# Kernel tuning notes

Measured on AMD Instinct MI355X. Metric: run time of the kernel, lower is better.

The kernel has to match this reference:

```python
import jax, jax.numpy as jnp
import numpy as np

N_HEADS = 16
DIM = 1024
DPH = DIM // N_HEADS  # 64
NEG_INF = -1e20       # neginf(float32) in the torch source


def setup_inputs() -> dict:
    key0 = jax.random.key(0)
    ks = jax.random.split(key0, 12)
    bs, qlen, nrev, klen = 32, 128, 20, 64
    w = lambda k: jax.random.normal(k, (DIM, DIM), jnp.float32) * 0.02
    return {
        "query": jax.random.normal(ks[0], (bs, qlen, DIM), jnp.float32),
        "key": jax.random.normal(ks[1], (bs, nrev, klen, DIM), jnp.float32),
        "value": jax.random.normal(ks[2], (bs, nrev, klen, DIM), jnp.float32),
        "mask": jax.random.randint(ks[3], (bs, nrev), 0, 2, jnp.int32),
        "mask2": jax.random.randint(ks[4], (bs, nrev, klen), 0, 2, jnp.int32),
        "Wq": w(ks[5]), "bq": jnp.zeros((DIM,), jnp.float32),
        "Wk": w(ks[6]), "bk": jnp.zeros((DIM,), jnp.float32),
        "Wv": w(ks[7]), "bv": jnp.zeros((DIM,), jnp.float32),
        "Wo": w(ks[8]), "bo": jnp.zeros((DIM,), jnp.float32),
        "sa_a": jax.random.normal(ks[9], (DPH, DPH), jnp.float32) * 0.1,
        "sa_b": jax.random.normal(ks[10], (DPH, 1), jnp.float32) * 0.1,
    }


def _forward(query, key, value, mask, mask2,
             Wq, bq, Wk, bk, Wv, bv, Wo, bo, sa_a, sa_b):
    bs, qlen, dim = query.shape
    _, nrev, klen, _ = key.shape
    dph = dim // N_HEADS
    scale = float(dph) ** 0.5

    # linear projections + head split (torch Linear: x @ W.T + b)
    q = (query @ Wq.T + bq).reshape(bs, qlen, N_HEADS, dph)        # [B,Q,H,d]
    k = (key @ Wk.T + bk).reshape(bs, nrev, klen, N_HEADS, dph)    # [B,R,T,H,d]
    v = (value @ Wv.T + bv).reshape(bs, nrev, klen, N_HEADS, dph)  # [B,R,T,H,d]

    # --- token-level attention: per review, q attends over review tokens ---
    scores = jnp.einsum('bqhd,brthd->bhrqt', q, k) / scale          # [B,H,R,Q,T]
    tok_pad = (mask2 == 0)[:, None, :, None, :]                     # [B,1,R,1,T]
    scores = jnp.where(tok_pad, NEG_INF, scores)
    attn_w = jax.nn.softmax(scores, axis=-1)
    att = jnp.einsum('bhrqt,brthd->bhqrd', attn_w, v)               # [B,H,Q,R,d]

    # --- review-level self-attention pooling (SelfAttentionSeq) ---
    # e = tanh(h @ a) @ b ; mask applied only if some reviews have mask==0,
    # and then NONZERO mask positions get -1e30 (faithful to the source).
    e = jnp.tanh(att @ sa_a) @ sa_b                                 # [B,H,Q,R,1]
    e = e[..., 0]                                                   # [B,H,Q,R]
    mf = mask.astype(att.dtype)                                     # [B,R]
    any_zero = (jnp.sum(mask == 0, axis=-1, keepdims=True) > 0).astype(att.dtype)  # [B,1]
    add_mask = (-1e30 * mf) * any_zero                              # [B,R]
    e = e + add_mask[:, None, None, :]
    rev_w = jax.nn.softmax(e, axis=-1)                              # [B,H,Q,R]
    pooled = jnp.einsum('bhqr,bhqrd->bhqd', rev_w, att)             # [B,H,Q,d]

    # merge heads + output projection
    merged = pooled.transpose(0, 2, 1, 3).reshape(bs, qlen, dim)    # [B,Q,D]
    return merged @ Wo.T + bo


def reference(query, key, value, mask, mask2,
              Wq, bq, Wk, bk, Wv, bv, Wo, bo, sa_a, sa_b):
    return _forward(query, key, value, mask, mask2,
                    Wq, bq, Wk, bk, Wv, bv, Wo, bo, sa_a, sa_b)
```

## Files before the change

### kernel.cpp

```cpp
#include <hip/hip_runtime.h>
#include <stdint.h>


typedef __attribute__((ext_vector_type(8))) short bf16x8;
typedef __attribute__((ext_vector_type(4))) float f32x4;
typedef __attribute__((ext_vector_type(4))) unsigned int u32x4;
typedef __attribute__((address_space(1))) const unsigned int as1_t;
typedef __attribute__((address_space(3))) unsigned int as3_t;

#define DEVI static __device__ __forceinline__

DEVI unsigned short f2bf(float f) {
  unsigned int u = __float_as_uint(f);
  u += 0x7fffu + ((u >> 16) & 1u);
  return (unsigned short)(u >> 16);
}
DEVI unsigned int pack2(float a, float b) {
  return (unsigned int)f2bf(a) | ((unsigned int)f2bf(b) << 16);
}
DEVI unsigned int cvtpk(float a, float b) {
  unsigned int r;
  asm("v_cvt_pk_bf16_f32 %0, %1, %2" : "=v"(r) : "v"(a), "v"(b));
  return r;
}

DEVI void gload_lds16(const void* g, void* l) {
  __builtin_amdgcn_global_load_lds((as1_t*)g, (as3_t*)l, 16, 0, 0);
}

DEVI float fast_tanh(float x) {
  float ax = fabsf(x);
  float e = __expf(2.0f * ax);
  float r = __builtin_fmaf(-2.0f, __builtin_amdgcn_rcpf(e + 1.0f), 1.0f);
  return copysignf(r, x);
}

__global__ __launch_bounds__(256) void prep(
    const float* __restrict__ w0, const float* __restrict__ w1,
    const float* __restrict__ w2, const float* __restrict__ w3,
    unsigned short* __restrict__ o0, unsigned short* __restrict__ o1,
    unsigned short* __restrict__ o2, unsigned short* __restrict__ o3,
    const float* __restrict__ qsrc, unsigned short* __restrict__ qdst,
    const int* __restrict__ mask, int* __restrict__ cmp) {
  const int bx = (int)blockIdx.x;
  const int tid = (int)threadIdx.x;
  if (bx < 1024) {
    const int i = bx * 256 + tid;
    f32x4 v;
    uint2 a;
    v = ((const f32x4*)w0)[i]; a.x = pack2(v[0], v[1]); a.y = pack2(v[2], v[3]);
    *(uint2*)(o0 + 4 * (size_t)i) = a;
    v = ((const f32x4*)w1)[i]; a.x = pack2(v[0], v[1]); a.y = pack2(v[2], v[3]);
    *(uint2*)(o1 + 4 * (size_t)i) = a;
    v = ((const f32x4*)w2)[i]; a.x = pack2(v[0], v[1]); a.y = pack2(v[2], v[3]);
    *(uint2*)(o2 + 4 * (size_t)i) = a;
    v = ((const f32x4*)w3)[i]; a.x = pack2(v[0], v[1]); a.y = pack2(v[2], v[3]);
    *(uint2*)(o3 + 4 * (size_t)i) = a;
  } else if (bx < 2048) {
    const int i = (bx - 1024) * 256 + tid;
#pragma unroll
    for (int h = 0; h < 2; ++h) {
      const int u = i + h * 262144;
      f32x4 a = ((const f32x4*)qsrc)[2 * u];
      f32x4 b = ((const f32x4*)qsrc)[2 * u + 1];
      u32x4 o = {pack2(a[0], a[1]), pack2(a[2], a[3]),
                 pack2(b[0], b[1]), pack2(b[2], b[3])};
      ((u32x4*)qdst)[u] = o;
    }
  } else {
    __shared__ int azs[32];
    if (tid < 32) {
      int z = 0;
#pragma unroll
      for (int r = 0; r < 20; ++r) z |= (mask[tid * 20 + r] == 0) ? 1 : 0;
      azs[tid] = z;
    }
    __syncthreads();
    if (tid < 64) {
      const int lane = tid;
      int base = 0;
      int lasts = 0;
      for (int it = 0; it < 10; ++it) {
        const int s = it * 64 + lane;
        const int bb = s / 20;
        const int actv = azs[bb] ? ((mask[s] == 0) ? 1 : 0) : 1;
        unsigned long long bal = __ballot(actv);
        const int off = (int)__popcll(bal & ((1ull << lane) - 1ull));
        if (actv) {
          cmp[1 + base + off] = s;
          lasts = s;
        }
        base += (int)__popcll(bal);
      }
#pragma unroll
      for (int d = 1; d < 64; d <<= 1) {
        int o = __shfl_xor(lasts, d);
        lasts = lasts > o ? lasts : o;
      }
      if (lane == 0) {
        cmp[0] = base;
        cmp[1 + base] = lasts;
      }
    }
  }
}

__global__ void cvt_act(const float* __restrict__ src,
                        unsigned short* __restrict__ dst,
                        const int* __restrict__ cmp) {
  const int cnt = cmp[0];
  const int n = ((cnt + 1) & ~1) * 8192;
  const int stride = (int)(gridDim.x * blockDim.x);
  for (int u = (int)(blockIdx.x * blockDim.x + threadIdx.x); u < n; u += stride) {
    const int s = u >> 13;
    const int e = u & 8191;
    const size_t so = (size_t)cmp[1 + s] * 65536 + (size_t)e * 8;
    f32x4 a = *(const f32x4*)(src + so);
    f32x4 b = *(const f32x4*)(src + so + 4);
    u32x4 o = {pack2(a[0], a[1]), pack2(a[2], a[3]),
               pack2(b[0], b[1]), pack2(b[2], b[3])};
    *(u32x4*)(dst + (size_t)u * 8) = o;
  }
}

template <int OUT_MODE, int ADT, int SC, int CMP>
__global__ __launch_bounds__(256, 4) void gemm_bt(
    const void* __restrict__ Ain, const unsigned short* __restrict__ W,
    const float* __restrict__ bias, void* __restrict__ Cout, int N, int K, int nnt,
    const int* __restrict__ cmp) {
  __shared__ __align__(16) char smem[32768];
  char* Asb = smem;
  char* Bsb = smem + 16384;
  const int tid = (int)threadIdx.x;
  const int lane = tid & 63, wave = tid >> 6;
  const int lm = lane & 15, l4 = lane >> 4;
  const int nb = (int)gridDim.x;
  const int bx = (int)blockIdx.x;
  const int wr = wave >> 1, wc = wave & 1;

  int mt, nt, cs0, cs1;
  if (CMP) {
    const int cnt = cmp[0];
    const int tiles = (cnt + 1) >> 1;
    if (bx >= tiles * 8) return;
    const int lg = (bx & 7) * tiles + (bx >> 3);
    mt = lg / nnt;
    nt = lg % nnt;
    cs0 = cmp[1 + 2 * mt];
    cs1 = cmp[2 + 2 * mt];
  } else {
    const int lg = (bx & 7) * (nb >> 3) + (bx >> 3);
    mt = lg / nnt;
    nt = lg % nnt;
    cs0 = 2 * mt;
    cs1 = 2 * mt + 1;
  }

  f32x4 zero4 = {0.f, 0.f, 0.f, 0.f};
  f32x4 acc[4][4];
#pragma unroll
  for (int i = 0; i < 4; ++i)
#pragma unroll
    for (int j = 0; j < 4; ++j) acc[i][j] = zero4;

  const int srow = tid >> 2, sblk = tid & 3;
  const int scb = sblk ^ ((srow >> 1) & 3);
  const unsigned short* wpg = W + (size_t)(nt * 128 + srow) * K + scb * 8;
  const int kx = (lm >> 1) & 3;

  const unsigned short* apg =
      (const unsigned short*)Ain + (size_t)(mt * 128 + srow) * K + scb * 8;
  const int NT = K >> 5;
#pragma unroll
  for (int t0 = 0; t0 < 2; ++t0) {
    const int kt = t0 * 32;
    gload_lds16(apg + kt, Asb + t0 * 8192 + tid * 16);
    gload_lds16(apg + (size_t)64 * K + kt, Asb + t0 * 8192 + 4096 + tid * 16);
    gload_lds16(wpg + kt, Bsb + t0 * 8192 + tid * 16);
    gload_lds16(wpg + (size_t)64 * K + kt, Bsb + t0 * 8192 + 4096 + tid * 16);
  }
  int cur = 0;
  for (int t = 0; t < NT; ++t) {
    if (t + 1 < NT)
      asm volatile("s_waitcnt vmcnt(4)" ::: "memory");
    else
      asm volatile("s_waitcnt vmcnt(0)" ::: "memory");
    asm volatile("s_barrier" ::: "memory");
    bf16x8 af[4], bfr[4];
#pragma unroll
    for (int i = 0; i < 4; ++i)
      af[i] = *(const bf16x8*)(Asb + cur * 8192 + (wr * 64 + i * 16 + lm) * 64 +
                               ((l4 ^ kx) * 16));
#pragma unroll
    for (int j = 0; j < 4; ++j)
      bfr[j] = *(const bf16x8*)(Bsb + cur * 8192 + (wc * 64 + j * 16 + lm) * 64 +
                                ((l4 ^ kx) * 16));
#pragma unroll
    for (int i = 0; i < 4; ++i)
#pragma unroll
      for (int j = 0; j < 4; ++j)
        acc[i][j] = __builtin_amdgcn_mfma_f32_16x16x32_bf16(af[i], bfr[j], acc[i][j], 0, 0, 0);
    asm volatile("s_barrier" ::: "memory");
    if (t + 2 < NT) {
      const int kt = (t + 2) * 32;
      gload_lds16(apg + kt, Asb + cur * 8192 + tid * 16);
      gload_lds16(apg + (size_t)64 * K + kt, Asb + cur * 8192 + 4096 + tid * 16);
      gload_lds16(wpg + kt, Bsb + cur * 8192 + tid * 16);
      gload_lds16(wpg + (size_t)64 * K + kt, Bsb + cur * 8192 + 4096 + tid * 16);
    }
    cur ^= 1;
  }

  const int c0o = nt * 128 + wc * 64 + lm;
  float bb[4];
#pragma unroll
  for (int j = 0; j < 4; ++j) bb[j] = bias[c0o + j * 16];
  const int mslot = wr ? cs1 : cs0;

  if (OUT_MODE < 2) {
#pragma unroll
    for (int i = 0; i < 4; ++i)
#pragma unroll
      for (int j = 0; j < 4; ++j)
#pragma unroll
        for (int p = 0; p < 4; ++p) {
          size_t grow = (size_t)mslot * 64 + (l4 * 4 + i * 16 + p);
          size_t idx = grow * N + (size_t)(c0o + j * 16);
          float v = acc[i][j][p] + bb[j];
          if (SC) v *= 0.125f;
          if (OUT_MODE == 1)
            ((unsigned short*)Cout)[idx] = f2bf(v);
          else
            ((float*)Cout)[idx] = v;
        }
  } else {
    const int hh = (nt * 128 + wc * 64) / 64;
    unsigned short* vt = (unsigned short*)Cout;
    const size_t base = ((size_t)mslot * 16 + hh) * 4096;
#pragma unroll
    for (int j = 0; j < 4; ++j) {
      const int d = lm + j * 16;
#pragma unroll
      for (int i = 0; i < 4; ++i) {
        uint2 wv;
        wv.x = pack2(acc[i][j][0] + bb[j], acc[i][j][1] + bb[j]);
        wv.y = pack2(acc[i][j][2] + bb[j], acc[i][j][3] + bb[j]);
        *(uint2*)(vt + base + (size_t)d * 64 + i * 16 + l4 * 4) = wv;
      }
    }
  }
}

__global__ __launch_bounds__(512, 4) void attn2(
    const unsigned short* __restrict__ qb, const unsigned short* __restrict__ kb,
    const unsigned short* __restrict__ vtg, const int* __restrict__ mask,
    const int* __restrict__ mask2, const float* __restrict__ sa_a,
    const float* __restrict__ sa_b, unsigned short* __restrict__ merged) {
  const int h = (int)blockIdx.x;
  const int b = (int)blockIdx.y;
  const int tid = (int)threadIdx.x;
  const int lane = tid & 63, wave = tid >> 6;
  const int lm = lane & 15, l4 = lane >> 4;
  const int sw = (lm & 7) << 4;

  __shared__ unsigned short kv_s[2][2][64 * 64];
  __shared__ unsigned short pa_s[8 * 16 * 64];

  char* kvb0 = (char*)kv_s;
  char* qreg = (char*)kv_s + 16384;
  char* satb = (char*)pa_s;

  unsigned am = 0u;
#pragma unroll
  for (int rr = 0; rr < 20; ++rr)
    am |= (mask[b * 20 + rr] == 0) ? (1u << rr) : 0u;
  const unsigned act = am ? am : 0xFFFFFu;

#pragma unroll
  for (int s = 0; s < 2; ++s) {
    int idx = s * 512 + tid, row = idx >> 3, blk = idx & 7;
    int cb = blk ^ (row & 7);
    gload_lds16(qb + (size_t)(b * 128 + row) * 1024 + h * 64 + cb * 8, qreg + idx * 16);
  }
#pragma unroll
  for (int s = 0; s < 8; ++s) {
    int idx = s * 512 + tid, jj = idx & 63, d = idx >> 6;
    *(unsigned short*)(satb + jj * 128 + ((d * 2) ^ ((jj & 7) << 4))) =
        f2bf(sa_a[d * 64 + jj]);
  }
  const int srow = tid >> 3, sblk = tid & 7;
  const int scb = sblk ^ (srow & 7);
  int r = (int)__builtin_ctz(act);
  unsigned rem = act & (act - 1u);
  gload_lds16(kb + ((size_t)(b * 20 + r) * 64 + srow) * 1024 + h * 64 + scb * 8,
              kvb0 + tid * 16);
  gload_lds16(vtg + ((size_t)(b * 20 + r) * 16 + h) * 4096 + srow * 64 + scb * 8,
              kvb0 + 8192 + tid * 16);

  f32x4 sbv[4];
#pragma unroll
  for (int i = 0; i < 4; ++i) sbv[i] = *(const f32x4*)(sa_b + i * 16 + l4 * 4);

  __syncthreads();

  const char* qrp = qreg + (wave * 16 + lm) * 128;
  bf16x8 qf[2];
  qf[0] = *(const bf16x8*)(qrp + ((l4 * 16) ^ sw));
  qf[1] = *(const bf16x8*)(qrp + ((64 + l4 * 16) ^ sw));
  bf16x8 sfr[2][4];
#pragma unroll
  for (int kk = 0; kk < 2; ++kk)
#pragma unroll
    for (int i = 0; i < 4; ++i)
      sfr[kk][i] = *(const bf16x8*)(satb + (i * 16 + lm) * 128 +
                                    ((kk * 64 + l4 * 16) ^ sw));
  asm volatile("s_waitcnt lgkmcnt(0)" ::: "memory");
  __syncthreads();

  char* pw = (char*)pa_s + wave * 2048 + lm * 128;

  f32x4 zero4 = {0.f, 0.f, 0.f, 0.f};
  f32x4 Pacc[4];
#pragma unroll
  for (int i = 0; i < 4; ++i) Pacc[i] = zero4;
  float m_run = -3.0e38f, s_run = 0.0f;

  int it = 0;
  for (;;) {
    const int pb = it & 1;
    if (it) __syncthreads();
    const int nr = rem ? (int)__builtin_ctz(rem) : -1;
    if (nr >= 0) {
      const int nbuf = pb ^ 1;
      gload_lds16(kb + ((size_t)(b * 20 + nr) * 64 + srow) * 1024 + h * 64 + scb * 8,
                  kvb0 + nbuf * 16384 + tid * 16);
      gload_lds16(vtg + ((size_t)(b * 20 + nr) * 16 + h) * 4096 + srow * 64 + scb * 8,
                  kvb0 + nbuf * 16384 + 8192 + tid * 16);
    }
    const char* kbse = kvb0 + pb * 16384;
    const char* vbse = kvb0 + pb * 16384 + 8192;

    const int mbase = (b * 20 + r) * 64;
    int4 m2v[4];
#pragma unroll
    for (int i = 0; i < 4; ++i)
      m2v[i] = *(const int4*)(mask2 + mbase + i * 16 + l4 * 4);

    f32x4 sc[4];
#pragma unroll
    for (int i = 0; i < 4; ++i) sc[i] = zero4;
    __builtin_amdgcn_s_setprio(1);
#pragma unroll
    for (int kk = 0; kk < 2; ++kk) {
      bf16x8 kf[4];
#pragma unroll
      for (int i = 0; i < 4; ++i)
        kf[i] = *(const bf16x8*)(kbse + (i * 16 + lm) * 128 + ((kk * 64 + l4 * 16) ^ sw));
#pragma unroll
      for (int i = 0; i < 4; ++i)
        sc[i] = __builtin_amdgcn_mfma_f32_16x16x32_bf16(kf[i], qf[kk], sc[i], 0, 0, 0);
    }
    __builtin_amdgcn_s_setprio(0);

#pragma unroll
    for (int i = 0; i < 4; ++i) {
      sc[i][0] = (m2v[i].x == 0) ? -1e20f : sc[i][0];
      sc[i][1] = (m2v[i].y == 0) ? -1e20f : sc[i][1];
      sc[i][2] = (m2v[i].z == 0) ? -1e20f : sc[i][2];
      sc[i][3] = (m2v[i].w == 0) ? -1e20f : sc[i][3];
    }
    float mx = sc[0][0];
#pragma unroll
    for (int i = 0; i < 4; ++i)
#pragma unroll
      for (int p = 0; p < 4; ++p) mx = fmaxf(mx, sc[i][p]);
    mx = fmaxf(mx, __shfl_xor(mx, 16));
    mx = fmaxf(mx, __shfl_xor(mx, 32));
    float sum = 0.f;
#pragma unroll
    for (int i = 0; i < 4; ++i)
#pragma unroll
      for (int p = 0; p < 4; ++p) {
        float e = __expf(sc[i][p] - mx);
        sc[i][p] = e;
        sum += e;
      }
    sum += __shfl_xor(sum, 16);
    sum += __shfl_xor(sum, 32);
    const float pinv = __builtin_amdgcn_rcpf(sum);

#pragma unroll
    for (int i = 0; i < 4; ++i) {
      uint2 wv;
      wv.x = cvtpk(sc[i][0] * pinv, sc[i][1] * pinv);
      wv.y = cvtpk(sc[i][2] * pinv, sc[i][3] * pinv);
      *(uint2*)(pw + ((i * 32 + l4 * 8) ^ sw)) = wv;
    }

    f32x4 av[4];
#pragma unroll
    for (int i = 0; i < 4; ++i) av[i] = zero4;
    __builtin_amdgcn_s_setprio(1);
#pragma unroll
    for (int kk = 0; kk < 2; ++kk) {
      bf16x8 pf = *(const bf16x8*)(pw + ((kk * 64 + l4 * 16) ^ sw));
      bf16x8 vf[4];
#pragma unroll
      for (int i = 0; i < 4; ++i)
        vf[i] = *(const bf16x8*)(vbse + (i * 16 + lm) * 128 + ((kk * 64 + l4 * 16) ^ sw));
#pragma unroll
      for (int i = 0; i < 4; ++i)
        av[i] = __builtin_amdgcn_mfma_f32_16x16x32_bf16(vf[i], pf, av[i], 0, 0, 0);
    }
    __builtin_amdgcn_s_setprio(0);

#pragma unroll
    for (int i = 0; i < 4; ++i) {
      uint2 wv;
      wv.x = cvtpk(av[i][0], av[i][1]);
      wv.y = cvtpk(av[i][2], av[i][3]);
      *(uint2*)(pw + ((i * 32 + l4 * 8) ^ sw)) = wv;
    }

    f32x4 ep[4];
#pragma unroll
    for (int i = 0; i < 4; ++i) ep[i] = zero4;
    __builtin_amdgcn_s_setprio(1);
#pragma unroll
    for (int kk = 0; kk < 2; ++kk) {
      bf16x8 afr = *(const bf16x8*)(pw + ((kk * 64 + l4 * 16) ^ sw));
#pragma unroll
      for (int i = 0; i < 4; ++i)
        ep[i] = __builtin_amdgcn_mfma_f32_16x16x32_bf16(sfr[kk][i], afr, ep[i], 0, 0, 0);
    }
    __builtin_amdgcn_s_setprio(0);
    float a = 0.f;
#pragma unroll
    for (int i = 0; i < 4; ++i)
#pragma unroll
      for (int p = 0; p < 4; ++p) a += fast_tanh(ep[i][p]) * sbv[i][p];
    a += __shfl_xor(a, 16);
    a += __shfl_xor(a, 32);

    const float e_r = a;
    const float mnew = fmaxf(m_run, e_r);
    const float scl = __expf(m_run - mnew);
    const float w = __expf(e_r - mnew);
    s_run = s_run * scl + w;
#pragma unroll
    for (int i = 0; i < 4; ++i)
#pragma unroll
      for (int p = 0; p < 4; ++p) Pacc[i][p] = Pacc[i][p] * scl + w * av[i][p];
    m_run = mnew;

    if (nr < 0) break;
    r = nr;
    rem &= rem - 1u;
    ++it;
  }

  const float inv_s = __builtin_amdgcn_rcpf(s_run);
  unsigned short* mrow = merged + (size_t)(b * 128 + wave * 16 + lm) * 1024 + h * 64;
#pragma unroll
  for (int i = 0; i < 4; ++i) {
    uint2 o;
    o.x = cvtpk(Pacc[i][0] * inv_s, Pacc[i][1] * inv_s);
    o.y = cvtpk(Pacc[i][2] * inv_s, Pacc[i][3] * inv_s);
    *(uint2*)(mrow + i * 16 + l4 * 4) = o;
  }
}

extern "C" void kernel_launch(void* const* d_in, const int* in_sizes, int n_in,
                              void* d_out, int out_size, void* d_ws, size_t ws_size,
                              hipStream_t stream) {
  (void)in_sizes; (void)n_in; (void)out_size; (void)ws_size;
  const float* query = (const float*)d_in[0];
  const float* key   = (const float*)d_in[1];
  const float* value = (const float*)d_in[2];
  const int*   mask  = (const int*)d_in[3];
  const int*   mask2 = (const int*)d_in[4];
  const float* Wq = (const float*)d_in[5];
  const float* bq = (const float*)d_in[6];
  const float* Wk = (const float*)d_in[7];
  const float* bk = (const float*)d_in[8];
  const float* Wv = (const float*)d_in[9];
  const float* bv = (const float*)d_in[10];
  const float* Wo = (const float*)d_in[11];
  const float* bo = (const float*)d_in[12];
  const float* sa_a = (const float*)d_in[13];
  const float* sa_b = (const float*)d_in[14];

  char* ws = (char*)d_ws;
  size_t off = 0;
  auto carve = [&](size_t bytes) -> char* {
    char* p = ws + off;
    off += (bytes + 255) & ~(size_t)255;
    return p;
  };
  unsigned short* wq_b = (unsigned short*)carve((size_t)1024 * 1024 * 2);
  unsigned short* wk_b = (unsigned short*)carve((size_t)1024 * 1024 * 2);
  unsigned short* wv_b = (unsigned short*)carve((size_t)1024 * 1024 * 2);
  unsigned short* wo_b = (unsigned short*)carve((size_t)1024 * 1024 * 2);
  unsigned short* q_b  = (unsigned short*)carve((size_t)4096 * 1024 * 2);
  unsigned short* k_b  = (unsigned short*)carve((size_t)40960 * 1024 * 2);
  unsigned short* vt_g = (unsigned short*)carve((size_t)40960 * 1024 * 2);
  unsigned short* mrg  = (unsigned short*)carve((size_t)4096 * 1024 * 2);
  int* cmp = (int*)carve(4096);
  unsigned short* act = (unsigned short*)carve((size_t)40960 * 1024 * 2);

  prep<<<2049, 256, 0, stream>>>(Wq, Wk, Wv, Wo, wq_b, wk_b, wv_b, wo_b,
                                 query, act, mask, cmp);

  gemm_bt<1, 1, 1, 0><<<dim3(32 * 8), 256, 0, stream>>>(act, wq_b, bq, q_b, 1024, 1024, 8, cmp);

  cvt_act<<<2048, 256, 0, stream>>>(key, act, cmp);
  gemm_bt<1, 1, 0, 1><<<dim3(320 * 8), 256, 0, stream>>>(act, wk_b, bk, k_b, 1024, 1024, 8, cmp);

  cvt_act<<<2048, 256, 0, stream>>>(value, act, cmp);
  gemm_bt<2, 1, 0, 1><<<dim3(320 * 8), 256, 0, stream>>>(act, wv_b, bv, vt_g, 1024, 1024, 8, cmp);

  attn2<<<dim3(16, 32), 512, 0, stream>>>(q_b, k_b, vt_g, mask, mask2, sa_a, sa_b, mrg);

  gemm_bt<0, 1, 0, 0><<<dim3(32 * 8), 256, 0, stream>>>(mrg, wo_b, bo, d_out, 1024, 1024, 8, cmp);
}
```

Baseline: 259.0 us.

## Fuse key conversion into prep, merge Q/K GEMMs, use sparse in-place activation layout

Active reviews are no longer compacted into a dense buffer. The key and value conversions now write bf16 rows in place at their original slot offsets and skip inactive reviews using a per-block mask bitmap. The GEMM gathers the two 64-row halves of each tile through the compacted slot list. The key conversion moves into the prep launch and the Q and K projections share one launch, which cuts kernel launches and lets the small Q GEMM overlap the K GEMM. The cost is a larger prep grid, a separate Q activation buffer, and a loop in which every thread iterates over all 640 slots even when most are inactive.

```diff
diff --git a/kernel.cpp b/kernel.cpp
--- a/kernel.cpp
+++ b/kernel.cpp
@@ -33,6 +33,34 @@
   float e = __expf(2.0f * ax);
   float r = __builtin_fmaf(-2.0f, __builtin_amdgcn_rcpf(e + 1.0f), 1.0f);
   return copysignf(r, x);
+}
+
+DEVI void cvt_sparse_body(const float* __restrict__ src,
+                          unsigned short* __restrict__ dst,
+                          const unsigned char* actb, int gid, int stride) {
+  for (int u = gid; u < 640 * 8192; u += stride) {
+    const int s = u >> 13;
+    if (!actb[s]) continue;
+    f32x4 a = *(const f32x4*)(src + (size_t)u * 8);
+    f32x4 b = *(const f32x4*)(src + (size_t)u * 8 + 4);
+    u32x4 o = {pack2(a[0], a[1]), pack2(a[2], a[3]),
+               pack2(b[0], b[1]), pack2(b[2], b[3])};
+    *(u32x4*)(dst + (size_t)u * 8) = o;
+  }
+}
+
+DEVI void build_actb(const int* __restrict__ mask, unsigned char* actb,
+                     int* azs, int tid) {
+  if (tid < 32) {
+    int z = 0;
+#pragma unroll
+    for (int r = 0; r < 20; ++r) z |= (mask[tid * 20 + r] == 0) ? 1 : 0;
+    azs[tid] = z;
+  }
+  __syncthreads();
+  for (int s = tid; s < 640; s += 256)
+    actb[s] = azs[s / 20] ? ((mask[s] == 0) ? 1 : 0) : 1;
+  __syncthreads();
 }
 
 __global__ __launch_bounds__(256) void prep(
@@ -41,6 +69,7 @@
     unsigned short* __restrict__ o0, unsigned short* __restrict__ o1,
     unsigned short* __restrict__ o2, unsigned short* __restrict__ o3,
     const float* __restrict__ qsrc, unsigned short* __restrict__ qdst,
+    const float* __restrict__ ksrc, unsigned short* __restrict__ kdst,
     const int* __restrict__ mask, int* __restrict__ cmp) {
   const int bx = (int)blockIdx.x;
   const int tid = (int)threadIdx.x;
@@ -67,7 +96,7 @@
                  pack2(b[0], b[1]), pack2(b[2], b[3])};
       ((u32x4*)qdst)[u] = o;
     }
-  } else {
+  } else if (bx == 2048) {
     __shared__ int azs[32];
     if (tid < 32) {
       int z = 0;
@@ -102,40 +131,36 @@
         cmp[1 + base] = lasts;
       }
     }
-  }
-}
-
-__global__ void cvt_act(const float* __restrict__ src,
-                        unsigned short* __restrict__ dst,
-                        const int* __restrict__ cmp) {
-  const int cnt = cmp[0];
-  const int n = ((cnt + 1) & ~1) * 8192;
-  const int stride = (int)(gridDim.x * blockDim.x);
-  for (int u = (int)(blockIdx.x * blockDim.x + threadIdx.x); u < n; u += stride) {
-    const int s = u >> 13;
-    const int e = u & 8191;
-    const size_t so = (size_t)cmp[1 + s] * 65536 + (size_t)e * 8;
-    f32x4 a = *(const f32x4*)(src + so);
-    f32x4 b = *(const f32x4*)(src + so + 4);
-    u32x4 o = {pack2(a[0], a[1]), pack2(a[2], a[3]),
-               pack2(b[0], b[1]), pack2(b[2], b[3])};
-    *(u32x4*)(dst + (size_t)u * 8) = o;
-  }
-}
-
-template <int OUT_MODE, int ADT, int SC, int CMP>
-__global__ __launch_bounds__(256, 4) void gemm_bt(
-    const void* __restrict__ Ain, const unsigned short* __restrict__ W,
-    const float* __restrict__ bias, void* __restrict__ Cout, int N, int K, int nnt,
-    const int* __restrict__ cmp) {
-  __shared__ __align__(16) char smem[32768];
+  } else {
+    __shared__ unsigned char actb[640];
+    __shared__ int azs[32];
+    build_actb(mask, actb, azs, tid);
+    cvt_sparse_body(ksrc, kdst, actb, (bx - 2049) * 256 + tid, 2048 * 256);
+  }
+}
+
+__global__ __launch_bounds__(256) void cvt_sp(const float* __restrict__ src,
+                                              unsigned short* __restrict__ dst,
+                                              const int* __restrict__ mask) {
+  __shared__ unsigned char actb[640];
+  __shared__ int azs[32];
+  const int tid = (int)threadIdx.x;
+  build_actb(mask, actb, azs, tid);
+  cvt_sparse_body(src, dst, actb, (int)(blockIdx.x * 256) + tid,
+                  (int)(gridDim.x * 256));
+}
+
+template <int OUT_MODE, int SC, int CMP>
+DEVI void gemm_body(const void* __restrict__ Ain,
+                    const unsigned short* __restrict__ W,
+                    const float* __restrict__ bias, void* __restrict__ Cout,
+                    int N, int K, int nnt, int nb, int bx,
+                    const int* __restrict__ cmp, char* smem) {
   char* Asb = smem;
   char* Bsb = smem + 16384;
   const int tid = (int)threadIdx.x;
   const int lane = tid & 63, wave = tid >> 6;
   const int lm = lane & 15, l4 = lane >> 4;
-  const int nb = (int)gridDim.x;
-  const int bx = (int)blockIdx.x;
   const int wr = wave >> 1, wc = wave & 1;
 
   int mt, nt, cs0, cs1;
@@ -168,14 +193,16 @@
   const unsigned short* wpg = W + (size_t)(nt * 128 + srow) * K + scb * 8;
   const int kx = (lm >> 1) & 3;
 
-  const unsigned short* apg =
-      (const unsigned short*)Ain + (size_t)(mt * 128 + srow) * K + scb * 8;
+  const unsigned short* apg0 =
+      (const unsigned short*)Ain + ((size_t)cs0 * 64 + srow) * K + scb * 8;
+  const unsigned short* apg1 =
+      (const unsigned short*)Ain + ((size_t)cs1 * 64 + srow) * K + scb * 8;
   const int NT = K >> 5;
 #pragma unroll
   for (int t0 = 0; t0 < 2; ++t0) {
     const int kt = t0 * 32;
-    gload_lds16(apg + kt, Asb + t0 * 8192 + tid * 16);
-    gload_lds16(apg + (size_t)64 * K + kt, Asb + t0 * 8192 + 4096 + tid * 16);
+    gload_lds16(apg0 + kt, Asb + t0 * 8192 + tid * 16);
+    gload_lds16(apg1 + kt, Asb + t0 * 8192 + 4096 + tid * 16);
     gload_lds16(wpg + kt, Bsb + t0 * 8192 + tid * 16);
     gload_lds16(wpg + (size_t)64 * K + kt, Bsb + t0 * 8192 + 4096 + tid * 16);
   }
@@ -203,8 +230,8 @@
     asm volatile("s_barrier" ::: "memory");
     if (t + 2 < NT) {
       const int kt = (t + 2) * 32;
-      gload_lds16(apg + kt, Asb + cur * 8192 + tid * 16);
-      gload_lds16(apg + (size_t)64 * K + kt, Asb + cur * 8192 + 4096 + tid * 16);
+      gload_lds16(apg0 + kt, Asb + cur * 8192 + tid * 16);
+      gload_lds16(apg1 + kt, Asb + cur * 8192 + 4096 + tid * 16);
       gload_lds16(wpg + kt, Bsb + cur * 8192 + tid * 16);
       gload_lds16(wpg + (size_t)64 * K + kt, Bsb + cur * 8192 + 4096 + tid * 16);
     }
@@ -249,6 +276,36 @@
       }
     }
   }
+}
+
+__global__ __launch_bounds__(256, 4) void gemm_qk(
+    const unsigned short* __restrict__ aq, const unsigned short* __restrict__ wq,
+    const float* __restrict__ bq, unsigned short* __restrict__ qout,
+    const unsigned short* __restrict__ ak, const unsigned short* __restrict__ wk,
+    const float* __restrict__ bk, unsigned short* __restrict__ kout,
+    const int* __restrict__ cmp) {
+  __shared__ __align__(16) char smem[32768];
+  const int bx = (int)blockIdx.x;
+  if (bx < 256)
+    gemm_body<1, 1, 0>(aq, wq, bq, qout, 1024, 1024, 8, 256, bx, cmp, smem);
+  else
+    gemm_body<1, 0, 1>(ak, wk, bk, kout, 1024, 1024, 8, 2560, bx - 256, cmp, smem);
+}
+
+__global__ __launch_bounds__(256, 4) void gemm_v(
+    const unsigned short* __restrict__ av, const unsigned short* __restrict__ wv,
+    const float* __restrict__ bv, unsigned short* __restrict__ vout,
+    const int* __restrict__ cmp) {
+  __shared__ __align__(16) char smem[32768];
+  gemm_body<2, 0, 1>(av, wv, bv, vout, 1024, 1024, 8, 2560, (int)blockIdx.x, cmp, smem);
+}
+
+__global__ __launch_bounds__(256, 4) void gemm_out(
+    const unsigned short* __restrict__ am, const unsigned short* __restrict__ wo,
+    const float* __restrict__ bo, float* __restrict__ oout,
+    const int* __restrict__ cmp) {
+  __shared__ __align__(16) char smem[32768];
+  gemm_body<0, 0, 0>(am, wo, bo, oout, 1024, 1024, 8, 256, (int)blockIdx.x, cmp, smem);
 }
 
 __global__ __launch_bounds__(512, 4) void attn2(
@@ -507,19 +564,18 @@
   unsigned short* mrg  = (unsigned short*)carve((size_t)4096 * 1024 * 2);
   int* cmp = (int*)carve(4096);
   unsigned short* act = (unsigned short*)carve((size_t)40960 * 1024 * 2);
-
-  prep<<<2049, 256, 0, stream>>>(Wq, Wk, Wv, Wo, wq_b, wk_b, wv_b, wo_b,
-                                 query, act, mask, cmp);
-
-  gemm_bt<1, 1, 1, 0><<<dim3(32 * 8), 256, 0, stream>>>(act, wq_b, bq, q_b, 1024, 1024, 8, cmp);
-
-  cvt_act<<<2048, 256, 0, stream>>>(key, act, cmp);
-  gemm_bt<1, 1, 0, 1><<<dim3(320 * 8), 256, 0, stream>>>(act, wk_b, bk, k_b, 1024, 1024, 8, cmp);
-
-  cvt_act<<<2048, 256, 0, stream>>>(value, act, cmp);
-  gemm_bt<2, 1, 0, 1><<<dim3(320 * 8), 256, 0, stream>>>(act, wv_b, bv, vt_g, 1024, 1024, 8, cmp);
+  unsigned short* act_q = (unsigned short*)carve((size_t)4096 * 1024 * 2);
+
+  prep<<<4097, 256, 0, stream>>>(Wq, Wk, Wv, Wo, wq_b, wk_b, wv_b, wo_b,
+                                 query, act_q, key, act, mask, cmp);
+
+  gemm_qk<<<256 + 2560, 256, 0, stream>>>(act_q, wq_b, bq, q_b,
+                                          act, wk_b, bk, k_b, cmp);
+
+  cvt_sp<<<2048, 256, 0, stream>>>(value, act, mask);
+  gemm_v<<<2560, 256, 0, stream>>>(act, wv_b, bv, vt_g, cmp);
 
   attn2<<<dim3(16, 32), 512, 0, stream>>>(q_b, k_b, vt_g, mask, mask2, sa_a, sa_b, mrg);
 
-  gemm_bt<0, 1, 0, 0><<<dim3(32 * 8), 256, 0, stream>>>(mrg, wo_b, bo, d_out, 1024, 1024, 8, cmp);
-}
+  gemm_out<<<256, 256, 0, stream>>>(mrg, wo_b, bo, (float*)d_out, cmp);
+}
```

Measured after the change: 255.0 us. No clear change (-1.6%).
